# Performance work log

Measured on AMD Instinct MI355X. Metric: run time of the kernel, lower is better.

Reference implementation:

```python
import jax, jax.numpy as jnp
import numpy as np

N_HEAD = 16
N_KV_HEAD = 4


def setup_inputs() -> dict:
    key = jax.random.key(0)
    ks = jax.random.split(key, 5)
    B, T, C = 2, 2048, 2048
    kv_dim = (C // N_HEAD) * N_KV_HEAD  # 512
    s = 0.02
    return {
        "x": jax.random.normal(ks[0], (B, T, C), dtype=jnp.float32),
        "Wq": jax.random.normal(ks[1], (C, C), dtype=jnp.float32) * s,
        "Wk": jax.random.normal(ks[2], (kv_dim, C), dtype=jnp.float32) * s,
        "Wv": jax.random.normal(ks[3], (kv_dim, C), dtype=jnp.float32) * s,
        "Wo": jax.random.normal(ks[4], (C, C), dtype=jnp.float32) * s,
    }


def reference(x, Wq, Wk, Wv, Wo):
    B, T, C = x.shape
    H, KV = N_HEAD, N_KV_HEAD
    hd = C // H          # 128
    g = H // KV          # query groups per kv head
    scale = hd ** -0.5

    # projections (torch Linear: y = x @ W.T)
    # q heads laid out so head h -> (kv = h // g, group j = h % g),
    # matching repeat_interleave(groups, dim=1) on k/v.
    q = (x @ Wq.T).reshape(B, T, KV, g, hd).transpose(0, 2, 3, 1, 4)  # [B,KV,g,T,hd]
    k = (x @ Wk.T).reshape(B, T, KV, hd).transpose(0, 2, 1, 3)        # [B,KV,T,hd]
    v = (x @ Wv.T).reshape(B, T, KV, hd).transpose(0, 2, 1, 3)        # [B,KV,T,hd]

    # GQA attention without materializing repeated KV heads
    att = jnp.einsum("bkgtd,bksd->bkgts", q, k) * scale  # [B,KV,g,T,T]
    causal = jnp.tril(jnp.ones((T, T), dtype=bool))
    att = jnp.where(causal, att, jnp.float32(-jnp.inf))
    att = jax.nn.softmax(att, axis=-1)
    # dropout p = config.dropout assumed 0 (eval/deterministic reference)

    out = jnp.einsum("bkgts,bksd->bkgtd", att, v)          # [B,KV,g,T,hd]
    out = out.transpose(0, 3, 1, 2, 4).reshape(B, T, C)    # [B,T,C]
    return out @ Wo.T
```

## Files before the change

kernel.cpp:

```cpp
#include <hip/hip_runtime.h>
#include <hip/hip_bf16.h>
#include <math.h>

typedef __bf16 bf16;
typedef __bf16 bf16x4 __attribute__((ext_vector_type(4)));
typedef __bf16 bf16x8 __attribute__((ext_vector_type(8)));
typedef float f32x4 __attribute__((ext_vector_type(4)));
typedef float f32x16 __attribute__((ext_vector_type(16)));
typedef unsigned int uint32x4 __attribute__((ext_vector_type(4)));

__device__ __forceinline__ void gload_lds16(const void* g, void* l) {
  __builtin_amdgcn_global_load_lds(
      (const __attribute__((address_space(1))) void*)g,
      (__attribute__((address_space(3))) void*)l, 16, 0, 0);
}

__device__ __forceinline__ unsigned int packbf(float a, float b) {
  union { bf16 h[2]; unsigned int u; } x;
  x.h[0] = (bf16)a; x.h[1] = (bf16)b;
  return x.u;
}

__global__ void cvt_all(const float* __restrict__ x,  const float* __restrict__ Wq,
                        const float* __restrict__ Wk, const float* __restrict__ Wv,
                        const float* __restrict__ Wo,
                        bf16* __restrict__ xb, bf16* __restrict__ wqkv, bf16* __restrict__ wob,
                        float qscale) {
  const int stride = gridDim.x * blockDim.x;
  const int total4 = 4718592;
  for (int i = blockIdx.x * blockDim.x + threadIdx.x; i < total4; i += stride) {
    const size_t e = (size_t)i * 4;
    const float* src; bf16* dst; size_t off; float sc = 1.f;
    if (e < 8388608)       { src = x;  dst = xb;            off = e; }
    else if (e < 12582912) { src = Wq; dst = wqkv;          off = e - 8388608; sc = qscale; }
    else if (e < 13631488) { src = Wk; dst = wqkv + 4194304; off = e - 12582912; }
    else if (e < 14680064) { src = Wv; dst = wqkv + 5242880; off = e - 13631488; }
    else                   { src = Wo; dst = wob;           off = e - 14680064; }
    float4 v = *(const float4*)(src + off);
    bf16x4 o;
    o[0] = (bf16)(v.x * sc); o[1] = (bf16)(v.y * sc);
    o[2] = (bf16)(v.z * sc); o[3] = (bf16)(v.w * sc);
    *(bf16x4*)(dst + off) = o;
  }
}

template <int MODE>
__global__ __launch_bounds__(256)
void gemm128(const bf16* __restrict__ A, const bf16* __restrict__ B,
             float* __restrict__ Cf, bf16* __restrict__ Qb, bf16* __restrict__ Kb,
             bf16* __restrict__ Vtb, int K, int Nst) {
  __shared__ __align__(16) char smem[32768];

  const int tid  = threadIdx.x;
  const int lane = tid & 63, w = tid >> 6;
  const int wr   = w >> 1, wc = w & 1;
  const int fr   = lane & 15, fq = lane >> 4;
  const int brow = blockIdx.y, bcol = blockIdx.x;

  f32x4 acc[4][4] = {};

  const bf16* Ab = A + (size_t)brow * 128 * K;
  const bf16* Bb = B + (size_t)bcol * 128 * K;
  const int NT = K >> 5;

  const int srow = w * 32 + (lane >> 2);
  const int skc  = (lane & 3) * 8;

  auto stage = [&](int t, int buf) {
    char* base = smem + buf * 16384;
    gload_lds16(Ab + (size_t)srow * K + t * 32 + skc,        base + w * 2048);
    gload_lds16(Ab + (size_t)(srow + 16) * K + t * 32 + skc, base + w * 2048 + 1024);
    gload_lds16(Bb + (size_t)srow * K + t * 32 + skc,        base + 8192 + w * 2048);
    gload_lds16(Bb + (size_t)(srow + 16) * K + t * 32 + skc, base + 8192 + w * 2048 + 1024);
  };

  stage(0, 0);
  for (int t = 0; t < NT; ++t) {
    const int buf = t & 1;
    if (t + 1 < NT) {
      stage(t + 1, buf ^ 1);
      asm volatile("s_waitcnt vmcnt(4)" ::: "memory");
    } else {
      asm volatile("s_waitcnt vmcnt(0)" ::: "memory");
    }
    __builtin_amdgcn_s_barrier();

    const char* pA = smem + buf * 16384;
    const char* pB = pA + 8192;
    bf16x8 af[4], bfr[4];
#pragma unroll
    for (int i = 0; i < 4; ++i) {
      af[i]  = *(const bf16x8*)(pA + ((wr * 64 + i * 16 + fr) * 64 + fq * 16));
      bfr[i] = *(const bf16x8*)(pB + ((wc * 64 + i * 16 + fr) * 64 + fq * 16));
    }
#pragma unroll
    for (int mi = 0; mi < 4; ++mi)
#pragma unroll
      for (int ni = 0; ni < 4; ++ni)
        acc[mi][ni] = __builtin_amdgcn_mfma_f32_16x16x32_bf16(af[mi], bfr[ni], acc[mi][ni], 0, 0, 0);
    __builtin_amdgcn_s_barrier();
  }

  const int r0 = brow * 128 + wr * 64 + fq * 4;
  const int c0 = bcol * 128 + wc * 64 + fr;
#pragma unroll
  for (int mi = 0; mi < 4; ++mi)
#pragma unroll
    for (int ni = 0; ni < 4; ++ni)
#pragma unroll
      for (int j = 0; j < 4; ++j) {
        const int r = r0 + mi * 16 + j;
        const int c = c0 + ni * 16;
        const float v = acc[mi][ni][j];
        if constexpr (MODE == 0) {
          Cf[(size_t)r * Nst + c] = v;
        } else {
          if (c < 2048)       Qb[(size_t)r * 2048 + c] = (bf16)v;
          else if (c < 2560)  Kb[(size_t)r * 512 + (c - 2048)] = (bf16)v;
          else                Vtb[(size_t)(c - 2560) * 4096 + r] = (bf16)v;
        }
      }
}

__global__ __launch_bounds__(256, 2)
void attn_fwd(const bf16* __restrict__ Q, const bf16* __restrict__ Kg_,
              const bf16* __restrict__ Vt, bf16* __restrict__ AO) {
  const int T = 2048, C = 2048, KVD = 512, MTOK = 4096;
  const int bid = blockIdx.x;
  const int qt  = (bid < 256) ? (15 - (bid >> 5)) : ((bid >> 5) - 8);
  const int sub = bid & 31;
  const int h = sub & 15, b = sub >> 4;
  const int kvh = h >> 2;
  const int lane = threadIdx.x & 63, w = threadIdx.x >> 6;
  const int hi = lane >> 5, lo = lane & 31;

  __shared__ __align__(16) char smem[65536];
  char* sK  = smem;
  char* sVt = smem + 32768;

  const bf16* Qg = Q   + (size_t)b * T * C + (size_t)h * 128;
  const bf16* Kg = Kg_ + (size_t)b * T * KVD + (size_t)kvh * 128;
  const bf16* Vg = Vt  + (size_t)kvh * 128 * MTOK + (size_t)b * T;

  const int q0 = qt * 128;
  const int qw = q0 + w * 32;

  bf16x8 qf[8];
#pragma unroll
  for (int ks = 0; ks < 8; ++ks)
    qf[ks] = *(const bf16x8*)(Qg + (size_t)(qw + lo) * C + ks * 16 + hi * 8);

  f32x16 ot[4] = {};
  float mstat = -INFINITY, lstat = 0.f;

  const int nt = 2 * qt + 2;

  auto stage = [&](int t, int buf) {
#pragma unroll
    for (int i = 0; i < 4; ++i) {
      const int ci = i * 256 + threadIdx.x;
      const int rk = ci >> 4, ck = ci & 15;
      gload_lds16(Kg + (size_t)(t * 64 + rk) * KVD + ((ck ^ (rk & 7)) * 8),
                  sK + buf * 16384 + i * 4096 + w * 1024);
      const int rv = ci >> 3, cv = ci & 7;
      gload_lds16(Vg + (size_t)rv * MTOK + t * 64 + ((cv ^ (rv & 7)) * 8),
                  sVt + buf * 16384 + i * 4096 + w * 1024);
    }
  };

  auto compute = [&](int t, int buf) {
    const int kv0 = t * 64;
    if (kv0 > qw + 31) return;
    const char* kb = sK + buf * 16384;
    const char* vb = sVt + buf * 16384;

    f32x16 sa[2] = {};
    __builtin_amdgcn_s_setprio(1);
#pragma unroll
    for (int ks = 0; ks < 8; ++ks) {
#pragma unroll
      for (int nb = 0; nb < 2; ++nb) {
        const int r = nb * 32 + lo;
        bf16x8 kf = *(const bf16x8*)(kb + (r * 256 + (((ks * 2 + hi) ^ (r & 7)) * 16)));
        sa[nb] = __builtin_amdgcn_mfma_f32_32x32x16_bf16(kf, qf[ks], sa[nb], 0, 0, 0);
      }
    }
    __builtin_amdgcn_s_setprio(0);
    if (kv0 + 63 > qw) {
      const int qg = qw + lo;
#pragma unroll
      for (int nb = 0; nb < 2; ++nb)
#pragma unroll
        for (int r = 0; r < 16; ++r) {
          const int kvg = kv0 + nb * 32 + (r & 3) + 8 * (r >> 2) + 4 * hi;
          if (kvg > qg) sa[nb][r] = -1e30f;
        }
    }
    float pm = -INFINITY;
#pragma unroll
    for (int nb = 0; nb < 2; ++nb)
#pragma unroll
      for (int r = 0; r < 16; ++r) pm = fmaxf(pm, sa[nb][r]);
    pm = fmaxf(pm, __shfl_xor(pm, 32));

    if (__any(pm > mstat + 8.f)) {
      const float mn = fmaxf(mstat, pm);
      const float rs = __expf(mstat - mn);
      mstat = mn;
      lstat *= rs;
#pragma unroll
      for (int db = 0; db < 4; ++db)
#pragma unroll
        for (int r = 0; r < 16; ++r) ot[db][r] *= rs;
    }

    float ls = 0.f;
    unsigned int pw[2][8];
#pragma unroll
    for (int nb = 0; nb < 2; ++nb)
#pragma unroll
      for (int j = 0; j < 8; ++j) {
        const float e0 = __expf(sa[nb][2 * j]     - mstat);
        const float e1 = __expf(sa[nb][2 * j + 1] - mstat);
        ls += e0 + e1;
        pw[nb][j] = packbf(e0, e1);
      }
    ls += __shfl_xor(ls, 32);
    lstat += ls;

#pragma unroll
    for (int nb = 0; nb < 2; ++nb) {
      unsigned int pj[8];
#pragma unroll
      for (int j = 0; j < 8; ++j) pj[j] = __shfl_xor(pw[nb][j], 32);
      __builtin_amdgcn_s_setprio(1);
#pragma unroll
      for (int half = 0; half < 2; ++half) {
        const int x = half * 4;
        uint32x4 bw;
        bw[0] = hi ? pj[x + 2] : pw[nb][x + 0];
        bw[1] = hi ? pj[x + 3] : pw[nb][x + 1];
        bw[2] = hi ? pw[nb][x + 2] : pj[x + 0];
        bw[3] = hi ? pw[nb][x + 3] : pj[x + 1];
        const bf16x8 pb = __builtin_bit_cast(bf16x8, bw);
        const int ks = nb * 2 + half;
#pragma unroll
        for (int db = 0; db < 4; ++db) {
          const int rv = db * 32 + lo;
          bf16x8 vf = *(const bf16x8*)(vb + (rv * 128 + (((ks * 2 + hi) ^ (rv & 7)) * 16)));
          ot[db] = __builtin_amdgcn_mfma_f32_32x32x16_bf16(vf, pb, ot[db], 0, 0, 0);
        }
      }
      __builtin_amdgcn_s_setprio(0);
    }
  };

  stage(0, 0);
  for (int t = 0; t < nt - 1; ++t) {
    stage(t + 1, (t + 1) & 1);
    asm volatile("s_waitcnt vmcnt(8)" ::: "memory");
    __builtin_amdgcn_s_barrier();
    compute(t, t & 1);
    __builtin_amdgcn_s_barrier();
  }
  asm volatile("s_waitcnt vmcnt(0)" ::: "memory");
  __builtin_amdgcn_s_barrier();
  compute(nt - 1, (nt - 1) & 1);

  __syncthreads();
  char* sO = smem;
  const float inv = 1.f / lstat;
  const int lq = w * 32 + lo;
#pragma unroll
  for (int db = 0; db < 4; ++db) {
#pragma unroll
    for (int j = 0; j < 8; ++j) {
      const int r = 2 * j;
      const int d = db * 32 + (r & 3) + 8 * (r >> 2) + 4 * hi;
      const unsigned int pv = packbf(ot[db][r] * inv, ot[db][r + 1] * inv);
      *(unsigned int*)(sO + (lq * 256 + ((2 * d) ^ (16 * (lq & 7))))) = pv;
    }
  }
  __syncthreads();
  bf16* Og = AO + (size_t)b * T * C + (size_t)h * 128;
#pragma unroll
  for (int i = 0; i < 8; ++i) {
    const int cid = i * 256 + threadIdx.x;
    const int rq = cid >> 4, c = cid & 15;
    bf16x8 vv = *(const bf16x8*)(sO + (rq * 256 + ((c * 16) ^ (16 * (rq & 7)))));
    *(bf16x8*)(Og + (size_t)(q0 + rq) * C + c * 8) = vv;
  }
}

extern "C" void kernel_launch(void* const* d_in, const int* in_sizes, int n_in,
                              void* d_out, int out_size, void* d_ws, size_t ws_size,
                              hipStream_t stream) {
  const float* x  = (const float*)d_in[0];
  const float* Wq = (const float*)d_in[1];
  const float* Wk = (const float*)d_in[2];
  const float* Wv = (const float*)d_in[3];
  const float* Wo = (const float*)d_in[4];
  float* out = (float*)d_out;

  char* ws = (char*)d_ws;
  bf16* xb   = (bf16*)(ws);
  bf16* wqkv = (bf16*)(ws + 16777216);
  bf16* wob  = (bf16*)(ws + 29360128);
  bf16* Qb   = (bf16*)(ws + 37748736);
  bf16* Kb   = (bf16*)(ws + 54525952);
  bf16* Vtb  = (bf16*)(ws + 58720256);
  bf16* AOb  = (bf16*)(ws + 62914560);

  const float scale = 0.08838834764831845f;
  cvt_all<<<2048, 256, 0, stream>>>(x, Wq, Wk, Wv, Wo, xb, wqkv, wob, scale);

  gemm128<1><<<dim3(24, 32), 256, 0, stream>>>(xb, wqkv, nullptr, Qb, Kb, Vtb, 2048, 0);

  attn_fwd<<<512, 256, 0, stream>>>(Qb, Kb, Vtb, AOb);

  gemm128<0><<<dim3(16, 32), 256, 0, stream>>>(AOb, wob, out, nullptr, nullptr, nullptr, 2048, 2048);
}
```

Baseline: 194.8 us.

## Single-buffer K in attention to cut LDS and allow three blocks per CU

K tiles are now held in a single LDS buffer while V stays double-buffered, which shrinks shared memory from 64KB to 48KB and raises launch bounds to allow three blocks per CU. The loop is restructured so the next K/V tile is prefetched after QK^T finishes and a barrier is passed, overlapping the load with softmax and PV. It waits for all loads at the end of each iteration, so there is less prefetch distance, and the tighter register budget may cause spills.

```diff
diff --git a/kernel.cpp b/kernel.cpp
--- a/kernel.cpp
+++ b/kernel.cpp
@@ -122,7 +122,7 @@
       }
 }
 
-__global__ __launch_bounds__(256, 2)
+__global__ __launch_bounds__(256, 3)
 void attn_fwd(const bf16* __restrict__ Q, const bf16* __restrict__ Kg_,
               const bf16* __restrict__ Vt, bf16* __restrict__ AO) {
   const int T = 2048, C = 2048, KVD = 512, MTOK = 4096;
@@ -134,9 +134,9 @@
   const int lane = threadIdx.x & 63, w = threadIdx.x >> 6;
   const int hi = lane >> 5, lo = lane & 31;
 
-  __shared__ __align__(16) char smem[65536];
+  __shared__ __align__(16) char smem[49152];
   char* sK  = smem;
-  char* sVt = smem + 32768;
+  char* sVt = smem + 16384;
 
   const bf16* Qg = Q   + (size_t)b * T * C + (size_t)h * 128;
   const bf16* Kg = Kg_ + (size_t)b * T * KVD + (size_t)kvh * 128;
@@ -155,119 +155,131 @@
 
   const int nt = 2 * qt + 2;
 
-  auto stage = [&](int t, int buf) {
+  auto stage_k = [&](int t) {
 #pragma unroll
     for (int i = 0; i < 4; ++i) {
       const int ci = i * 256 + threadIdx.x;
       const int rk = ci >> 4, ck = ci & 15;
       gload_lds16(Kg + (size_t)(t * 64 + rk) * KVD + ((ck ^ (rk & 7)) * 8),
-                  sK + buf * 16384 + i * 4096 + w * 1024);
+                  sK + i * 4096 + w * 1024);
+    }
+  };
+  auto stage_v = [&](int t, int buf) {
+#pragma unroll
+    for (int i = 0; i < 4; ++i) {
+      const int ci = i * 256 + threadIdx.x;
       const int rv = ci >> 3, cv = ci & 7;
       gload_lds16(Vg + (size_t)rv * MTOK + t * 64 + ((cv ^ (rv & 7)) * 8),
                   sVt + buf * 16384 + i * 4096 + w * 1024);
     }
   };
 
-  auto compute = [&](int t, int buf) {
-    const int kv0 = t * 64;
-    if (kv0 > qw + 31) return;
-    const char* kb = sK + buf * 16384;
-    const char* vb = sVt + buf * 16384;
-
-    f32x16 sa[2] = {};
-    __builtin_amdgcn_s_setprio(1);
-#pragma unroll
-    for (int ks = 0; ks < 8; ++ks) {
-#pragma unroll
-      for (int nb = 0; nb < 2; ++nb) {
-        const int r = nb * 32 + lo;
-        bf16x8 kf = *(const bf16x8*)(kb + (r * 256 + (((ks * 2 + hi) ^ (r & 7)) * 16)));
-        sa[nb] = __builtin_amdgcn_mfma_f32_32x32x16_bf16(kf, qf[ks], sa[nb], 0, 0, 0);
-      }
-    }
-    __builtin_amdgcn_s_setprio(0);
-    if (kv0 + 63 > qw) {
-      const int qg = qw + lo;
-#pragma unroll
-      for (int nb = 0; nb < 2; ++nb)
-#pragma unroll
-        for (int r = 0; r < 16; ++r) {
-          const int kvg = kv0 + nb * 32 + (r & 3) + 8 * (r >> 2) + 4 * hi;
-          if (kvg > qg) sa[nb][r] = -1e30f;
-        }
-    }
-    float pm = -INFINITY;
-#pragma unroll
-    for (int nb = 0; nb < 2; ++nb)
-#pragma unroll
-      for (int r = 0; r < 16; ++r) pm = fmaxf(pm, sa[nb][r]);
-    pm = fmaxf(pm, __shfl_xor(pm, 32));
-
-    if (__any(pm > mstat + 8.f)) {
-      const float mn = fmaxf(mstat, pm);
-      const float rs = __expf(mstat - mn);
-      mstat = mn;
-      lstat *= rs;
-#pragma unroll
-      for (int db = 0; db < 4; ++db)
-#pragma unroll
-        for (int r = 0; r < 16; ++r) ot[db][r] *= rs;
-    }
-
-    float ls = 0.f;
-    unsigned int pw[2][8];
-#pragma unroll
-    for (int nb = 0; nb < 2; ++nb)
-#pragma unroll
-      for (int j = 0; j < 8; ++j) {
-        const float e0 = __expf(sa[nb][2 * j]     - mstat);
-        const float e1 = __expf(sa[nb][2 * j + 1] - mstat);
-        ls += e0 + e1;
-        pw[nb][j] = packbf(e0, e1);
-      }
-    ls += __shfl_xor(ls, 32);
-    lstat += ls;
-
-#pragma unroll
-    for (int nb = 0; nb < 2; ++nb) {
-      unsigned int pj[8];
-#pragma unroll
-      for (int j = 0; j < 8; ++j) pj[j] = __shfl_xor(pw[nb][j], 32);
-      __builtin_amdgcn_s_setprio(1);
-#pragma unroll
-      for (int half = 0; half < 2; ++half) {
-        const int x = half * 4;
-        uint32x4 bw;
-        bw[0] = hi ? pj[x + 2] : pw[nb][x + 0];
-        bw[1] = hi ? pj[x + 3] : pw[nb][x + 1];
-        bw[2] = hi ? pw[nb][x + 2] : pj[x + 0];
-        bw[3] = hi ? pw[nb][x + 3] : pj[x + 1];
-        const bf16x8 pb = __builtin_bit_cast(bf16x8, bw);
-        const int ks = nb * 2 + half;
-#pragma unroll
-        for (int db = 0; db < 4; ++db) {
-          const int rv = db * 32 + lo;
-          bf16x8 vf = *(const bf16x8*)(vb + (rv * 128 + (((ks * 2 + hi) ^ (rv & 7)) * 16)));
-          ot[db] = __builtin_amdgcn_mfma_f32_32x32x16_bf16(vf, pb, ot[db], 0, 0, 0);
-        }
-      }
-      __builtin_amdgcn_s_setprio(0);
-    }
-  };
-
-  stage(0, 0);
-  for (int t = 0; t < nt - 1; ++t) {
-    stage(t + 1, (t + 1) & 1);
-    asm volatile("s_waitcnt vmcnt(8)" ::: "memory");
-    __builtin_amdgcn_s_barrier();
-    compute(t, t & 1);
-    __builtin_amdgcn_s_barrier();
-  }
+  stage_k(0);
+  stage_v(0, 0);
   asm volatile("s_waitcnt vmcnt(0)" ::: "memory");
   __builtin_amdgcn_s_barrier();
-  compute(nt - 1, (nt - 1) & 1);
-
-  __syncthreads();
+
+  for (int t = 0; t < nt; ++t) {
+    const int kv0 = t * 64;
+    const int buf = t & 1;
+    const bool live = (kv0 <= qw + 31);
+
+    f32x16 sa[2] = {};
+    if (live) {
+      __builtin_amdgcn_s_setprio(1);
+#pragma unroll
+      for (int ks = 0; ks < 8; ++ks) {
+#pragma unroll
+        for (int nb = 0; nb < 2; ++nb) {
+          const int r = nb * 32 + lo;
+          bf16x8 kf = *(const bf16x8*)(sK + (r * 256 + (((ks * 2 + hi) ^ (r & 7)) * 16)));
+          sa[nb] = __builtin_amdgcn_mfma_f32_32x32x16_bf16(kf, qf[ks], sa[nb], 0, 0, 0);
+        }
+      }
+      __builtin_amdgcn_s_setprio(0);
+    }
+    __builtin_amdgcn_s_barrier();
+
+    if (t + 1 < nt) {
+      stage_k(t + 1);
+      stage_v(t + 1, buf ^ 1);
+    }
+
+    if (live) {
+      if (kv0 + 63 > qw) {
+        const int qg = qw + lo;
+#pragma unroll
+        for (int nb = 0; nb < 2; ++nb)
+#pragma unroll
+          for (int r = 0; r < 16; ++r) {
+            const int kvg = kv0 + nb * 32 + (r & 3) + 8 * (r >> 2) + 4 * hi;
+            if (kvg > qg) sa[nb][r] = -1e30f;
+          }
+      }
+      float pm = -INFINITY;
+#pragma unroll
+      for (int nb = 0; nb < 2; ++nb)
+#pragma unroll
+        for (int r = 0; r < 16; ++r) pm = fmaxf(pm, sa[nb][r]);
+      pm = fmaxf(pm, __shfl_xor(pm, 32));
+
+      if (__any(pm > mstat + 8.f)) {
+        const float mn = fmaxf(mstat, pm);
+        const float rs = __expf(mstat - mn);
+        mstat = mn;
+        lstat *= rs;
+#pragma unroll
+        for (int db = 0; db < 4; ++db)
+#pragma unroll
+          for (int r = 0; r < 16; ++r) ot[db][r] *= rs;
+      }
+
+      float ls = 0.f;
+      unsigned int pw[2][8];
+#pragma unroll
+      for (int nb = 0; nb < 2; ++nb)
+#pragma unroll
+        for (int j = 0; j < 8; ++j) {
+          const float e0 = __expf(sa[nb][2 * j]     - mstat);
+          const float e1 = __expf(sa[nb][2 * j + 1] - mstat);
+          ls += e0 + e1;
+          pw[nb][j] = packbf(e0, e1);
+        }
+      ls += __shfl_xor(ls, 32);
+      lstat += ls;
+
+      const char* vb = sVt + buf * 16384;
+#pragma unroll
+      for (int nb = 0; nb < 2; ++nb) {
+        unsigned int pj[8];
+#pragma unroll
+        for (int j = 0; j < 8; ++j) pj[j] = __shfl_xor(pw[nb][j], 32);
+        __builtin_amdgcn_s_setprio(1);
+#pragma unroll
+        for (int half = 0; half < 2; ++half) {
+          const int x = half * 4;
+          uint32x4 bw;
+          bw[0] = hi ? pj[x + 2] : pw[nb][x + 0];
+          bw[1] = hi ? pj[x + 3] : pw[nb][x + 1];
+          bw[2] = hi ? pw[nb][x + 2] : pj[x + 0];
+          bw[3] = hi ? pw[nb][x + 3] : pj[x + 1];
+          const bf16x8 pb = __builtin_bit_cast(bf16x8, bw);
+          const int ks = nb * 2 + half;
+#pragma unroll
+          for (int db = 0; db < 4; ++db) {
+            const int rv = db * 32 + lo;
+            bf16x8 vf = *(const bf16x8*)(vb + (rv * 128 + (((ks * 2 + hi) ^ (rv & 7)) * 16)));
+            ot[db] = __builtin_amdgcn_mfma_f32_32x32x16_bf16(vf, pb, ot[db], 0, 0, 0);
+          }
+        }
+        __builtin_amdgcn_s_setprio(0);
+      }
+    }
+
+    asm volatile("s_waitcnt vmcnt(0)" ::: "memory");
+    __builtin_amdgcn_s_barrier();
+  }
+
   char* sO = smem;
   const float inv = 1.f / lstat;
   const int lq = w * 32 + lo;
```

Measured after the change: 204.1 us. 1.05x slower.

## Use 2 waves per attention block, each handling 64 query rows

Applied to the files above, without the earlier changes.

The attention kernel now runs with 128 threads instead of 256. Each wave processes two 32-row query sub-tiles, so every K and V fragment read from LDS feeds two MFMAs. This cuts LDS read traffic per FLOP but doubles accumulator and Q-fragment registers per wave, which may lower occupancy. It also means fewer waves are available to hide latency while the same 64KB of shared memory per block is kept.

```diff
diff --git a/kernel.cpp b/kernel.cpp
--- a/kernel.cpp
+++ b/kernel.cpp
@@ -122,7 +122,7 @@
       }
 }
 
-__global__ __launch_bounds__(256, 2)
+__global__ __launch_bounds__(128)
 void attn_fwd(const bf16* __restrict__ Q, const bf16* __restrict__ Kg_,
               const bf16* __restrict__ Vt, bf16* __restrict__ AO) {
   const int T = 2048, C = 2048, KVD = 512, MTOK = 4096;
@@ -131,7 +131,8 @@
   const int sub = bid & 31;
   const int h = sub & 15, b = sub >> 4;
   const int kvh = h >> 2;
-  const int lane = threadIdx.x & 63, w = threadIdx.x >> 6;
+  const int tid = threadIdx.x;
+  const int lane = tid & 63, w = tid >> 6;
   const int hi = lane >> 5, lo = lane & 31;
 
   __shared__ __align__(16) char smem[65536];
@@ -143,38 +144,44 @@
   const bf16* Vg = Vt  + (size_t)kvh * 128 * MTOK + (size_t)b * T;
 
   const int q0 = qt * 128;
-  const int qw = q0 + w * 32;
-
-  bf16x8 qf[8];
-#pragma unroll
-  for (int ks = 0; ks < 8; ++ks)
-    qf[ks] = *(const bf16x8*)(Qg + (size_t)(qw + lo) * C + ks * 16 + hi * 8);
-
-  f32x16 ot[4] = {};
-  float mstat = -INFINITY, lstat = 0.f;
+  const int qw = q0 + w * 64;
+
+  bf16x8 qf[2][8];
+#pragma unroll
+  for (int qi = 0; qi < 2; ++qi)
+#pragma unroll
+    for (int ks = 0; ks < 8; ++ks)
+      qf[qi][ks] = *(const bf16x8*)(Qg + (size_t)(qw + qi * 32 + lo) * C + ks * 16 + hi * 8);
+
+  f32x16 ot[2][4] = {};
+  float mstat[2] = {-INFINITY, -INFINITY}, lstat[2] = {0.f, 0.f};
 
   const int nt = 2 * qt + 2;
 
   auto stage = [&](int t, int buf) {
 #pragma unroll
-    for (int i = 0; i < 4; ++i) {
-      const int ci = i * 256 + threadIdx.x;
+    for (int i = 0; i < 8; ++i) {
+      const int ci = i * 128 + tid;
       const int rk = ci >> 4, ck = ci & 15;
       gload_lds16(Kg + (size_t)(t * 64 + rk) * KVD + ((ck ^ (rk & 7)) * 8),
-                  sK + buf * 16384 + i * 4096 + w * 1024);
+                  sK + buf * 16384 + i * 2048 + w * 1024);
+    }
+#pragma unroll
+    for (int i = 0; i < 8; ++i) {
+      const int ci = i * 128 + tid;
       const int rv = ci >> 3, cv = ci & 7;
       gload_lds16(Vg + (size_t)rv * MTOK + t * 64 + ((cv ^ (rv & 7)) * 8),
-                  sVt + buf * 16384 + i * 4096 + w * 1024);
+                  sVt + buf * 16384 + i * 2048 + w * 1024);
     }
   };
 
   auto compute = [&](int t, int buf) {
     const int kv0 = t * 64;
-    if (kv0 > qw + 31) return;
+    if (kv0 > qw + 63) return;
     const char* kb = sK + buf * 16384;
     const char* vb = sVt + buf * 16384;
 
-    f32x16 sa[2] = {};
+    f32x16 sa[2][2] = {};
     __builtin_amdgcn_s_setprio(1);
 #pragma unroll
     for (int ks = 0; ks < 8; ++ks) {
@@ -182,73 +189,92 @@
       for (int nb = 0; nb < 2; ++nb) {
         const int r = nb * 32 + lo;
         bf16x8 kf = *(const bf16x8*)(kb + (r * 256 + (((ks * 2 + hi) ^ (r & 7)) * 16)));
-        sa[nb] = __builtin_amdgcn_mfma_f32_32x32x16_bf16(kf, qf[ks], sa[nb], 0, 0, 0);
+        sa[0][nb] = __builtin_amdgcn_mfma_f32_32x32x16_bf16(kf, qf[0][ks], sa[0][nb], 0, 0, 0);
+        sa[1][nb] = __builtin_amdgcn_mfma_f32_32x32x16_bf16(kf, qf[1][ks], sa[1][nb], 0, 0, 0);
       }
     }
     __builtin_amdgcn_s_setprio(0);
     if (kv0 + 63 > qw) {
-      const int qg = qw + lo;
+#pragma unroll
+      for (int qi = 0; qi < 2; ++qi) {
+        const int qg = qw + qi * 32 + lo;
+#pragma unroll
+        for (int nb = 0; nb < 2; ++nb)
+#pragma unroll
+          for (int r = 0; r < 16; ++r) {
+            const int kvg = kv0 + nb * 32 + (r & 3) + 8 * (r >> 2) + 4 * hi;
+            if (kvg > qg) sa[qi][nb][r] = -1e30f;
+          }
+      }
+    }
+    float pm[2];
+#pragma unroll
+    for (int qi = 0; qi < 2; ++qi) {
+      float v = -INFINITY;
 #pragma unroll
       for (int nb = 0; nb < 2; ++nb)
 #pragma unroll
-        for (int r = 0; r < 16; ++r) {
-          const int kvg = kv0 + nb * 32 + (r & 3) + 8 * (r >> 2) + 4 * hi;
-          if (kvg > qg) sa[nb][r] = -1e30f;
+        for (int r = 0; r < 16; ++r) v = fmaxf(v, sa[qi][nb][r]);
+      v = fmaxf(v, __shfl_xor(v, 32));
+      pm[qi] = v;
+    }
+    if (__any((pm[0] > mstat[0] + 8.f) || (pm[1] > mstat[1] + 8.f))) {
+#pragma unroll
+      for (int qi = 0; qi < 2; ++qi) {
+        const float mn = fmaxf(mstat[qi], pm[qi]);
+        const float rs = __expf(mstat[qi] - mn);
+        mstat[qi] = mn;
+        lstat[qi] *= rs;
+#pragma unroll
+        for (int db = 0; db < 4; ++db)
+#pragma unroll
+          for (int r = 0; r < 16; ++r) ot[qi][db][r] *= rs;
+      }
+    }
+    unsigned int pw_[2][2][8];
+#pragma unroll
+    for (int qi = 0; qi < 2; ++qi) {
+      float ls = 0.f;
+#pragma unroll
+      for (int nb = 0; nb < 2; ++nb)
+#pragma unroll
+        for (int j = 0; j < 8; ++j) {
+          const float e0 = __expf(sa[qi][nb][2 * j]     - mstat[qi]);
+          const float e1 = __expf(sa[qi][nb][2 * j + 1] - mstat[qi]);
+          ls += e0 + e1;
+          pw_[qi][nb][j] = packbf(e0, e1);
         }
-    }
-    float pm = -INFINITY;
-#pragma unroll
-    for (int nb = 0; nb < 2; ++nb)
-#pragma unroll
-      for (int r = 0; r < 16; ++r) pm = fmaxf(pm, sa[nb][r]);
-    pm = fmaxf(pm, __shfl_xor(pm, 32));
-
-    if (__any(pm > mstat + 8.f)) {
-      const float mn = fmaxf(mstat, pm);
-      const float rs = __expf(mstat - mn);
-      mstat = mn;
-      lstat *= rs;
-#pragma unroll
-      for (int db = 0; db < 4; ++db)
-#pragma unroll
-        for (int r = 0; r < 16; ++r) ot[db][r] *= rs;
-    }
-
-    float ls = 0.f;
-    unsigned int pw[2][8];
-#pragma unroll
-    for (int nb = 0; nb < 2; ++nb)
-#pragma unroll
-      for (int j = 0; j < 8; ++j) {
-        const float e0 = __expf(sa[nb][2 * j]     - mstat);
-        const float e1 = __expf(sa[nb][2 * j + 1] - mstat);
-        ls += e0 + e1;
-        pw[nb][j] = packbf(e0, e1);
-      }
-    ls += __shfl_xor(ls, 32);
-    lstat += ls;
-
+      ls += __shfl_xor(ls, 32);
+      lstat[qi] += ls;
+    }
 #pragma unroll
     for (int nb = 0; nb < 2; ++nb) {
-      unsigned int pj[8];
-#pragma unroll
-      for (int j = 0; j < 8; ++j) pj[j] = __shfl_xor(pw[nb][j], 32);
+      unsigned int pj[2][8];
+#pragma unroll
+      for (int qi = 0; qi < 2; ++qi)
+#pragma unroll
+        for (int j = 0; j < 8; ++j) pj[qi][j] = __shfl_xor(pw_[qi][nb][j], 32);
       __builtin_amdgcn_s_setprio(1);
 #pragma unroll
       for (int half = 0; half < 2; ++half) {
         const int x = half * 4;
-        uint32x4 bw;
-        bw[0] = hi ? pj[x + 2] : pw[nb][x + 0];
-        bw[1] = hi ? pj[x + 3] : pw[nb][x + 1];
-        bw[2] = hi ? pw[nb][x + 2] : pj[x + 0];
-        bw[3] = hi ? pw[nb][x + 3] : pj[x + 1];
-        const bf16x8 pb = __builtin_bit_cast(bf16x8, bw);
+        bf16x8 pb[2];
+#pragma unroll
+        for (int qi = 0; qi < 2; ++qi) {
+          uint32x4 bw;
+          bw[0] = hi ? pj[qi][x + 2] : pw_[qi][nb][x + 0];
+          bw[1] = hi ? pj[qi][x + 3] : pw_[qi][nb][x + 1];
+          bw[2] = hi ? pw_[qi][nb][x + 2] : pj[qi][x + 0];
+          bw[3] = hi ? pw_[qi][nb][x + 3] : pj[qi][x + 1];
+          pb[qi] = __builtin_bit_cast(bf16x8, bw);
+        }
         const int ks = nb * 2 + half;
 #pragma unroll
         for (int db = 0; db < 4; ++db) {
           const int rv = db * 32 + lo;
           bf16x8 vf = *(const bf16x8*)(vb + (rv * 128 + (((ks * 2 + hi) ^ (rv & 7)) * 16)));
-          ot[db] = __builtin_amdgcn_mfma_f32_32x32x16_bf16(vf, pb, ot[db], 0, 0, 0);
+          ot[0][db] = __builtin_amdgcn_mfma_f32_32x32x16_bf16(vf, pb[0], ot[0][db], 0, 0, 0);
+          ot[1][db] = __builtin_amdgcn_mfma_f32_32x32x16_bf16(vf, pb[1], ot[1][db], 0, 0, 0);
         }
       }
       __builtin_amdgcn_s_setprio(0);
@@ -258,7 +284,7 @@
   stage(0, 0);
   for (int t = 0; t < nt - 1; ++t) {
     stage(t + 1, (t + 1) & 1);
-    asm volatile("s_waitcnt vmcnt(8)" ::: "memory");
+    asm volatile("s_waitcnt vmcnt(16)" ::: "memory");
     __builtin_amdgcn_s_barrier();
     compute(t, t & 1);
     __builtin_amdgcn_s_barrier();
@@ -269,23 +295,25 @@
 
   __syncthreads();
   char* sO = smem;
-  const float inv = 1.f / lstat;
-  const int lq = w * 32 + lo;
-#pragma unroll
-  for (int db = 0; db < 4; ++db) {
-#pragma unroll
-    for (int j = 0; j < 8; ++j) {
-      const int r = 2 * j;
-      const int d = db * 32 + (r & 3) + 8 * (r >> 2) + 4 * hi;
-      const unsigned int pv = packbf(ot[db][r] * inv, ot[db][r + 1] * inv);
-      *(unsigned int*)(sO + (lq * 256 + ((2 * d) ^ (16 * (lq & 7))))) = pv;
-    }
+#pragma unroll
+  for (int qi = 0; qi < 2; ++qi) {
+    const float inv = 1.f / lstat[qi];
+    const int lq = w * 64 + qi * 32 + lo;
+#pragma unroll
+    for (int db = 0; db < 4; ++db)
+#pragma unroll
+      for (int j = 0; j < 8; ++j) {
+        const int r = 2 * j;
+        const int d = db * 32 + (r & 3) + 8 * (r >> 2) + 4 * hi;
+        const unsigned int pv = packbf(ot[qi][db][r] * inv, ot[qi][db][r + 1] * inv);
+        *(unsigned int*)(sO + (lq * 256 + ((2 * d) ^ (16 * (lq & 7))))) = pv;
+      }
   }
   __syncthreads();
   bf16* Og = AO + (size_t)b * T * C + (size_t)h * 128;
 #pragma unroll
-  for (int i = 0; i < 8; ++i) {
-    const int cid = i * 256 + threadIdx.x;
+  for (int i = 0; i < 16; ++i) {
+    const int cid = i * 128 + tid;
     const int rq = cid >> 4, c = cid & 15;
     bf16x8 vv = *(const bf16x8*)(sO + (rq * 256 + ((c * 16) ^ (16 * (rq & 7)))));
     *(bf16x8*)(Og + (size_t)(q0 + rq) * C + c * 8) = vv;
@@ -316,7 +344,7 @@
 
   gemm128<1><<<dim3(24, 32), 256, 0, stream>>>(xb, wqkv, nullptr, Qb, Kb, Vtb, 2048, 0);
 
-  attn_fwd<<<512, 256, 0, stream>>>(Qb, Kb, Vtb, AOb);
+  attn_fwd<<<512, 128, 0, stream>>>(Qb, Kb, Vtb, AOb);
 
   gemm128<0><<<dim3(16, 32), 256, 0, stream>>>(AOb, wob, out, nullptr, nullptr, nullptr, 2048, 2048);
 }
```

After: 242.6 us. +24.5%, slower.
